# Optimization experiments

Measured on AMD Instinct MI355X. Metric: run time of the kernel, lower is better.

Reference implementation:

```python
import jax, jax.numpy as jnp
import numpy as np

H = 16          # num_attention_heads
D = 1024        # hidden_size
HD = D // H     # attention_head_size = 64


def setup_inputs() -> dict:
    key = jax.random.key(0)
    ks = jax.random.split(key, 9)
    s = 1.0 / np.sqrt(D)
    return {
        "hidden_states": jax.random.normal(ks[0], (4, 1024, D), jnp.float32),
        "encoder_hidden_states": jax.random.normal(ks[1], (4, 1024, D), jnp.float32),
        "attention_mask": jnp.zeros((4, 1, 1, 2048), jnp.float32),
        "Wq": jax.random.normal(ks[2], (D, D), jnp.float32) * s,
        "bq": jnp.zeros((D,), jnp.float32),
        "Wk": jax.random.normal(ks[3], (D, D), jnp.float32) * s,
        "bk": jnp.zeros((D,), jnp.float32),
        "Wv": jax.random.normal(ks[4], (D, D), jnp.float32) * s,
        "bv": jnp.zeros((D,), jnp.float32),
    }


def _split_heads(x):
    # [B, S, D] -> [B, H, S, HD]
    B, S, _ = x.shape
    return x.reshape(B, S, H, HD).transpose(0, 2, 1, 3)


def reference(hidden_states, encoder_hidden_states, attention_mask, Wq, bq, Wk, bk, Wv, bv):
    # KV over concat(encoder, decoder); Q over decoder hidden states only.
    all_hidden = jnp.concatenate([encoder_hidden_states, hidden_states], axis=1)  # [B, Skv, D]
    q = _split_heads(hidden_states @ Wq + bq)        # [B, H, Sq, HD]
    k = _split_heads(all_hidden @ Wk + bk)           # [B, H, Skv, HD]
    v = _split_heads(all_hidden @ Wv + bv)           # [B, H, Skv, HD]

    scores = jnp.einsum("bhqd,bhkd->bhqk", q, k) / np.sqrt(HD).astype(np.float32)
    scores = scores + attention_mask                 # additive mask, broadcast
    probs = jax.nn.softmax(scores, axis=-1)          # dropout p=0 (eval)
    ctx = jnp.einsum("bhqk,bhkd->bhqd", probs, v)    # [B, H, Sq, HD]
    B, _, Sq, _ = ctx.shape
    return ctx.transpose(0, 2, 1, 3).reshape(B, Sq, D)
```

## Files before the change

### kernel.cpp

```cpp
#include <hip/hip_runtime.h>


typedef _Float16 f16;
typedef __attribute__((ext_vector_type(4))) _Float16 half4;
typedef __attribute__((ext_vector_type(8))) _Float16 half8;
typedef __attribute__((ext_vector_type(4))) float floatx4;
typedef __attribute__((ext_vector_type(16))) float floatx16;
typedef __attribute__((ext_vector_type(4))) unsigned int uint4v;

#define GLOAD16(gp, lp)                                                        \
    __builtin_amdgcn_global_load_lds(                                          \
        (const __attribute__((address_space(1))) void*)(gp),                   \
        (__attribute__((address_space(3))) void*)(lp), 16, 0, 0)

__global__ void prep_kernel(const float* __restrict__ hid, const float* __restrict__ enc,
                            const float* __restrict__ Wq, const float* __restrict__ Wk,
                            const float* __restrict__ Wv, f16* __restrict__ Wtq,
                            f16* __restrict__ Wtk, f16* __restrict__ Wtv,
                            f16* __restrict__ Aall) {
    int bid = blockIdx.x, tid = threadIdx.x;
    if (bid < 3072) {
        __shared__ float tile[32][33];
        int z = bid >> 10, xy = bid & 1023;
        const float* W = (z == 0) ? Wq : (z == 1) ? Wk : Wv;
        f16* Wt = (z == 0) ? Wtq : (z == 1) ? Wtk : Wtv;
        int n0 = (xy & 31) * 32, k0 = (xy >> 5) * 32;
        int tx = tid & 31, ty = tid >> 5;
        #pragma unroll
        for (int i = 0; i < 32; i += 8)
            tile[ty + i][tx] = W[(k0 + ty + i) * 1024 + n0 + tx];
        __syncthreads();
        #pragma unroll
        for (int i = 0; i < 32; i += 8)
            Wt[(n0 + ty + i) * 1024 + k0 + tx] = (f16)tile[tx][ty + i];
    } else {
        int t = (bid - 3072) * 256 + tid;
        int rowg = t >> 7, col = (t & 127) * 8;
        int b = rowg >> 11, r = rowg & 2047;
        const float* src = (r < 1024 ? enc + ((size_t)b * 1024 + r) * 1024
                                     : hid + ((size_t)b * 1024 + (r - 1024)) * 1024) + col;
        float4 v0 = *(const float4*)src, v1 = *(const float4*)(src + 4);
        half8 o;
        o[0] = (f16)v0.x; o[1] = (f16)v0.y; o[2] = (f16)v0.z; o[3] = (f16)v0.w;
        o[4] = (f16)v1.x; o[5] = (f16)v1.y; o[6] = (f16)v1.z; o[7] = (f16)v1.w;
        *(half8*)(Aall + (size_t)rowg * 1024 + col) = o;
    }
}

__launch_bounds__(256)
__global__ void qkv_gemm(const f16* __restrict__ Aall,
                         const f16* __restrict__ Wtq, const f16* __restrict__ Wtk,
                         const f16* __restrict__ Wtv,
                         const float* __restrict__ bq, const float* __restrict__ bk,
                         const float* __restrict__ bv,
                         f16* __restrict__ Qw, f16* __restrict__ Kw, f16* __restrict__ Vtw) {
    int mode = blockIdx.z;
    if (mode == 0 && blockIdx.x >= 32) return;
    __shared__ f16 As0[128 * 32];
    __shared__ f16 Bs0[128 * 32];
    __shared__ f16 As1[128 * 32];
    __shared__ f16 Bs1[128 * 32];

    const f16* Wt = (mode == 0) ? Wtq : (mode == 1) ? Wtk : Wtv;
    const float* bias = (mode == 0) ? bq : (mode == 1) ? bk : bv;
    f16* out = (mode == 0) ? Qw : (mode == 1) ? Kw : Vtw;

    int tid = threadIdx.x;
    int m0 = blockIdx.x * 128, n0 = blockIdx.y * 128;
    int wid = tid >> 6, lane = tid & 63;
    int wm = (wid >> 1) * 64, wn = (wid & 1) * 64;
    int lr = lane & 15, lg = lane >> 4;

    floatx4 acc[4][4];
    #pragma unroll
    for (int i = 0; i < 4; i++)
        #pragma unroll
        for (int j = 0; j < 4; j++) acc[i][j] = (floatx4)(0.f);

    int trow = tid >> 2;
    int tcol = (((tid & 3) ^ ((tid >> 3) & 3))) * 8;
    const f16 *a0g, *a1g;
    {
        int mA0 = m0 + trow, mA1 = mA0 + 64;
        if (mode == 0) {
            int b0 = mA0 >> 10, b1 = mA1 >> 10;
            a0g = Aall + ((size_t)(b0 * 2048 + 1024 + (mA0 & 1023))) * 1024 + tcol;
            a1g = Aall + ((size_t)(b1 * 2048 + 1024 + (mA1 & 1023))) * 1024 + tcol;
        } else {
            a0g = Aall + (size_t)mA0 * 1024 + tcol;
            a1g = Aall + (size_t)mA1 * 1024 + tcol;
        }
    }
    const f16* b0g = Wt + (size_t)(n0 + trow) * 1024 + tcol;
    const f16* b1g = Wt + (size_t)(n0 + trow + 64) * 1024 + tcol;

    int rcol = (lg ^ ((lr >> 1) & 3)) * 8;

    GLOAD16(a0g, &As0[tid * 8]);
    GLOAD16(a1g, &As0[tid * 8 + 2048]);
    GLOAD16(b0g, &Bs0[tid * 8]);
    GLOAD16(b1g, &Bs0[tid * 8 + 2048]);
    GLOAD16(a0g + 32, &As1[tid * 8]);
    GLOAD16(a1g + 32, &As1[tid * 8 + 2048]);
    GLOAD16(b0g + 32, &Bs1[tid * 8]);
    GLOAD16(b1g + 32, &Bs1[tid * 8 + 2048]);
    asm volatile("s_waitcnt vmcnt(4)" ::: "memory");
    __builtin_amdgcn_s_barrier();

    #define QKV_COMPUTE(Abuf, Bbuf)                                                       \
        {                                                                                 \
            half8 a[4], bf[4];                                                            \
            _Pragma("unroll")                                                             \
            for (int i = 0; i < 4; i++)                                                   \
                a[i] = *(const half8*)&Abuf[(wm + i * 16 + lr) * 32 + rcol];              \
            _Pragma("unroll")                                                             \
            for (int j = 0; j < 4; j++)                                                   \
                bf[j] = *(const half8*)&Bbuf[(wn + j * 16 + lr) * 32 + rcol];             \
            __builtin_amdgcn_s_setprio(1);                                                \
            _Pragma("unroll")                                                             \
            for (int i = 0; i < 4; i++)                                                   \
                _Pragma("unroll")                                                         \
                for (int j = 0; j < 4; j++)                                               \
                    acc[i][j] = __builtin_amdgcn_mfma_f32_16x16x32_f16(a[i], bf[j],       \
                                                                      acc[i][j], 0, 0, 0);\
            __builtin_amdgcn_s_setprio(0);                                                \
        }

    for (int k0 = 0; k0 < 1024; k0 += 64) {
        QKV_COMPUTE(As0, Bs0);
        asm volatile("s_waitcnt lgkmcnt(0)" ::: "memory");
        __builtin_amdgcn_s_barrier();
        if (k0 + 64 < 1024) {
            GLOAD16(a0g + k0 + 64, &As0[tid * 8]);
            GLOAD16(a1g + k0 + 64, &As0[tid * 8 + 2048]);
            GLOAD16(b0g + k0 + 64, &Bs0[tid * 8]);
            GLOAD16(b1g + k0 + 64, &Bs0[tid * 8 + 2048]);
            asm volatile("s_waitcnt vmcnt(4)" ::: "memory");
        } else {
            asm volatile("s_waitcnt vmcnt(0)" ::: "memory");
        }
        __builtin_amdgcn_s_barrier();

        QKV_COMPUTE(As1, Bs1);
        asm volatile("s_waitcnt lgkmcnt(0)" ::: "memory");
        __builtin_amdgcn_s_barrier();
        if (k0 + 96 < 1024) {
            GLOAD16(a0g + k0 + 96, &As1[tid * 8]);
            GLOAD16(a1g + k0 + 96, &As1[tid * 8 + 2048]);
            GLOAD16(b0g + k0 + 96, &Bs1[tid * 8]);
            GLOAD16(b1g + k0 + 96, &Bs1[tid * 8 + 2048]);
            asm volatile("s_waitcnt vmcnt(4)" ::: "memory");
            __builtin_amdgcn_s_barrier();
        }
    }
    #undef QKV_COMPUTE

    if (mode == 2) {
        #pragma unroll
        for (int i = 0; i < 4; i++) {
            int mbase = m0 + wm + i * 16 + lg * 4;
            int b = mbase >> 11, s = mbase & 2047;
            #pragma unroll
            for (int j = 0; j < 4; j++) {
                int n = n0 + wn + j * 16 + lr;
                int h = n >> 6, d = n & 63;
                float bv = bias[n];
                half4 w;
                #pragma unroll
                for (int r = 0; r < 4; r++) w[r] = (f16)(acc[i][j][r] + bv);
                *(half4*)(out + ((size_t)((b * 16 + h) * 64 + d)) * 2048 + s) = w;
            }
        }
    } else {
        int Sout = (mode == 0) ? 1024 : 2048;
        #pragma unroll
        for (int i = 0; i < 4; i++) {
            int mbase = m0 + wm + i * 16 + lg * 4;
            #pragma unroll
            for (int j = 0; j < 4; j++) {
                int n = n0 + wn + j * 16 + lr;
                int h = n >> 6, d = n & 63;
                float bv = bias[n];
                #pragma unroll
                for (int r = 0; r < 4; r++) {
                    int m = mbase + r;
                    int b = (mode == 0) ? (m >> 10) : (m >> 11);
                    int s = (mode == 0) ? (m & 1023) : (m & 2047);
                    out[((size_t)(b * 16 + h) * Sout + s) * 64 + d] = (f16)(acc[i][j][r] + bv);
                }
            }
        }
    }
}

__device__ inline half8 pack_swap(float s0, float s1, float s2, float s3,
                                  float s4, float s5, float s6, float s7) {
    unsigned a0 = __builtin_bit_cast(unsigned, __builtin_amdgcn_cvt_pkrtz(s0, s1));
    unsigned b0 = __builtin_bit_cast(unsigned, __builtin_amdgcn_cvt_pkrtz(s4, s5));
    unsigned a1 = __builtin_bit_cast(unsigned, __builtin_amdgcn_cvt_pkrtz(s2, s3));
    unsigned b1 = __builtin_bit_cast(unsigned, __builtin_amdgcn_cvt_pkrtz(s6, s7));
    asm("v_permlane32_swap_b32 %0, %1" : "+v"(a0), "+v"(b0));
    asm("v_permlane32_swap_b32 %0, %1" : "+v"(a1), "+v"(b1));
    uint4v w = {a0, a1, b0, b1};
    return __builtin_bit_cast(half8, w);
}

__device__ inline half8 pack_noswap(float s0, float s1, float s2, float s3,
                                    float s4, float s5, float s6, float s7) {
    unsigned w0 = __builtin_bit_cast(unsigned, __builtin_amdgcn_cvt_pkrtz(s0, s1));
    unsigned w1 = __builtin_bit_cast(unsigned, __builtin_amdgcn_cvt_pkrtz(s2, s3));
    unsigned w2 = __builtin_bit_cast(unsigned, __builtin_amdgcn_cvt_pkrtz(s4, s5));
    unsigned w3 = __builtin_bit_cast(unsigned, __builtin_amdgcn_cvt_pkrtz(s6, s7));
    uint4v w = {w0, w1, w2, w3};
    return __builtin_bit_cast(half8, w);
}

__launch_bounds__(256)
__global__ void attn_kernel(const f16* __restrict__ Q, const f16* __restrict__ K,
                            const f16* __restrict__ Vt, const float* __restrict__ mask,
                            float* __restrict__ out) {
    __shared__ f16 Kt[2][64 * 72];
    __shared__ f16 Vtt[2][64 * 72];
    __shared__ float maskLds[2048];

    const float LOG2E = 1.4426950408889634f;
    int tid = threadIdx.x;
    int wid = tid >> 6, lane = tid & 63;
    int l31 = lane & 31, l5 = lane >> 5;

    int bid = blockIdx.x + 8 * blockIdx.y;
    int xcd = bid & 7, w = bid >> 3;
    int bh = xcd * 8 + (w >> 3);
    int xblk = w & 7;
    int b = bh >> 4;
    int q = xblk * 128 + wid * 32 + l31;

    half8 pa, pcode;
    #pragma unroll
    for (int j = 0; j < 8; j++) { pa[j] = (f16)0; pcode[j] = (f16)(8 * l5 + j); }
    if (l31 < 16 && (l31 >> 3) == l5) pa[l31 & 7] = (f16)1;
    floatx16 pd = __builtin_amdgcn_mfma_f32_32x32x16_f16(pa, pcode, (floatx16)0.f, 0, 0, 0);
    float r4 = __shfl(pd[0], 32);
    bool twoblk = (r4 > 6.0f);

    const float* maskp = mask + b * 2048;
    for (int i = tid; i < 512; i += 256) {
        float4 mv = ((const float4*)maskp)[i];
        mv.x = mv.x * LOG2E - 8.0f; mv.y = mv.y * LOG2E - 8.0f;
        mv.z = mv.z * LOG2E - 8.0f; mv.w = mv.w * LOG2E - 8.0f;
        ((float4*)maskLds)[i] = mv;
    }

    const f16* qrow = Q + ((size_t)bh * 1024 + q) * 64;
    half8 qf[4];
    if (!twoblk) {
        #pragma unroll
        for (int ks = 0; ks < 4; ks++)
            qf[ks] = *(const half8*)(qrow + ks * 16 + l5 * 8);
    } else {
        #pragma unroll
        for (int ks = 0; ks < 4; ks++) {
            half4 lo = *(const half4*)(qrow + ks * 16 + 4 * l5);
            half4 hi = *(const half4*)(qrow + ks * 16 + 8 + 4 * l5);
            qf[ks][0] = lo[0]; qf[ks][1] = lo[1]; qf[ks][2] = lo[2]; qf[ks][3] = lo[3];
            qf[ks][4] = hi[0]; qf[ks][5] = hi[1]; qf[ks][6] = hi[2]; qf[ks][7] = hi[3];
        }
    }
    const f16 qs = (f16)(0.125f * 1.4426950408889634f);
    #pragma unroll
    for (int ks = 0; ks < 4; ks++)
        #pragma unroll
        for (int x = 0; x < 8; x++) qf[ks][x] *= qs;

    half8 aones;
    #pragma unroll
    for (int j = 0; j < 8; j++) aones[j] = (l31 == 0) ? (f16)1 : (f16)0;

    floatx16 o0 = (floatx16)0.f, o1 = (floatx16)0.f, o2 = (floatx16)0.f;

    int sr = tid >> 2, sc = (tid & 3) * 16;
    const f16* Ksrc = K + ((size_t)bh * 2048 + sr) * 64 + sc;
    const f16* Vsrc = Vt + ((size_t)(bh * 64 + sr)) * 2048 + sc;

    half8 rk0 = *(const half8*)(Ksrc);
    half8 rk1 = *(const half8*)(Ksrc + 8);
    half8 rv0 = *(const half8*)(Vsrc);
    half8 rv1 = *(const half8*)(Vsrc + 8);
    *(half8*)&Kt[0][sr * 72 + sc]      = rk0;
    *(half8*)&Kt[0][sr * 72 + sc + 8]  = rk1;
    *(half8*)&Vtt[0][sr * 72 + sc]     = rv0;
    *(half8*)&Vtt[0][sr * 72 + sc + 8] = rv1;
    rk0 = *(const half8*)(Ksrc + (size_t)64 * 64);
    rk1 = *(const half8*)(Ksrc + (size_t)64 * 64 + 8);
    rv0 = *(const half8*)(Vsrc + 64);
    rv1 = *(const half8*)(Vsrc + 64 + 8);
    __syncthreads();

    int cur = 0;
    for (int kv0 = 0; kv0 < 2048; kv0 += 64) {
        if (kv0 < 2048 - 64) {
            int nx = cur ^ 1;
            *(half8*)&Kt[nx][sr * 72 + sc]      = rk0;
            *(half8*)&Kt[nx][sr * 72 + sc + 8]  = rk1;
            *(half8*)&Vtt[nx][sr * 72 + sc]     = rv0;
            *(half8*)&Vtt[nx][sr * 72 + sc + 8] = rv1;
            if (kv0 < 2048 - 128) {
                rk0 = *(const half8*)(Ksrc + (size_t)(kv0 + 128) * 64);
                rk1 = *(const half8*)(Ksrc + (size_t)(kv0 + 128) * 64 + 8);
                rv0 = *(const half8*)(Vsrc + kv0 + 128);
                rv1 = *(const half8*)(Vsrc + kv0 + 128 + 8);
            }
        }

        floatx16 sf0, sf1;
        #pragma unroll
        for (int g = 0; g < 4; g++) {
            float4 mk0 = *(const float4*)&maskLds[kv0 + 8 * g + 4 * l5];
            float4 mk1 = *(const float4*)&maskLds[kv0 + 32 + 8 * g + 4 * l5];
            #pragma unroll
            for (int i = 0; i < 4; i++) {
                sf0[4 * g + i] = ((const float*)&mk0)[i];
                sf1[4 * g + i] = ((const float*)&mk1)[i];
            }
        }

        __builtin_amdgcn_s_setprio(1);
        #pragma unroll
        for (int ks = 0; ks < 4; ks++) {
            half8 k0 = *(const half8*)&Kt[cur][l31 * 72 + ks * 16 + l5 * 8];
            half8 k1 = *(const half8*)&Kt[cur][(32 + l31) * 72 + ks * 16 + l5 * 8];
            sf0 = __builtin_amdgcn_mfma_f32_32x32x16_f16(k0, qf[ks], sf0, 0, 0, 0);
            sf1 = __builtin_amdgcn_mfma_f32_32x32x16_f16(k1, qf[ks], sf1, 0, 0, 0);
        }
        __builtin_amdgcn_s_setprio(0);

        #pragma unroll
        for (int r = 0; r < 16; r++) {
            sf0[r] = exp2f(sf0[r]);
            sf1[r] = exp2f(sf1[r]);
        }

        half8 pb[4];
        if (!twoblk) {
            pb[0] = pack_swap(sf0[0], sf0[1], sf0[2], sf0[3], sf0[4], sf0[5], sf0[6], sf0[7]);
            pb[1] = pack_swap(sf0[8], sf0[9], sf0[10], sf0[11], sf0[12], sf0[13], sf0[14], sf0[15]);
            pb[2] = pack_swap(sf1[0], sf1[1], sf1[2], sf1[3], sf1[4], sf1[5], sf1[6], sf1[7]);
            pb[3] = pack_swap(sf1[8], sf1[9], sf1[10], sf1[11], sf1[12], sf1[13], sf1[14], sf1[15]);
        } else {
            pb[0] = pack_noswap(sf0[0], sf0[1], sf0[2], sf0[3], sf0[4], sf0[5], sf0[6], sf0[7]);
            pb[1] = pack_noswap(sf0[8], sf0[9], sf0[10], sf0[11], sf0[12], sf0[13], sf0[14], sf0[15]);
            pb[2] = pack_noswap(sf1[0], sf1[1], sf1[2], sf1[3], sf1[4], sf1[5], sf1[6], sf1[7]);
            pb[3] = pack_noswap(sf1[8], sf1[9], sf1[10], sf1[11], sf1[12], sf1[13], sf1[14], sf1[15]);
        }

        __builtin_amdgcn_s_setprio(1);
        #pragma unroll
        for (int kb = 0; kb < 4; kb++) {
            half8 v0 = *(const half8*)&Vtt[cur][l31 * 72 + kb * 16 + l5 * 8];
            half8 v1 = *(const half8*)&Vtt[cur][(32 + l31) * 72 + kb * 16 + l5 * 8];
            o0 = __builtin_amdgcn_mfma_f32_32x32x16_f16(v0, pb[kb], o0, 0, 0, 0);
            o1 = __builtin_amdgcn_mfma_f32_32x32x16_f16(v1, pb[kb], o1, 0, 0, 0);
            o2 = __builtin_amdgcn_mfma_f32_32x32x16_f16(aones, pb[kb], o2, 0, 0, 0);
        }
        __builtin_amdgcn_s_setprio(0);

        asm volatile("s_waitcnt lgkmcnt(0)" ::: "memory");
        __builtin_amdgcn_sched_barrier(0);
        __builtin_amdgcn_s_barrier();
        cur ^= 1;
    }

    float l_all = __shfl(o2[0], l31);
    int h = bh & 15;
    float inv = 1.f / l_all;
    float* orow = out + ((size_t)(b * 1024 + q)) * 1024 + h * 64;
    #pragma unroll
    for (int g = 0; g < 4; g++) {
        float4 r0 = {o0[4 * g] * inv, o0[4 * g + 1] * inv, o0[4 * g + 2] * inv, o0[4 * g + 3] * inv};
        float4 r1 = {o1[4 * g] * inv, o1[4 * g + 1] * inv, o1[4 * g + 2] * inv, o1[4 * g + 3] * inv};
        *(float4*)&orow[8 * g + 4 * l5]      = r0;
        *(float4*)&orow[32 + 8 * g + 4 * l5] = r1;
    }
}

extern "C" void kernel_launch(void* const* d_in, const int* in_sizes, int n_in,
                              void* d_out, int out_size, void* d_ws, size_t ws_size,
                              hipStream_t stream) {
    const float* hid  = (const float*)d_in[0];
    const float* enc  = (const float*)d_in[1];
    const float* mask = (const float*)d_in[2];
    const float* Wq   = (const float*)d_in[3];
    const float* bq   = (const float*)d_in[4];
    const float* Wk   = (const float*)d_in[5];
    const float* bk   = (const float*)d_in[6];
    const float* Wv   = (const float*)d_in[7];
    const float* bv   = (const float*)d_in[8];
    float* out = (float*)d_out;

    char* ws = (char*)d_ws;
    f16* Wtq  = (f16*)(ws + ((size_t)0 << 20));
    f16* Wtk  = (f16*)(ws + ((size_t)2 << 20));
    f16* Wtv  = (f16*)(ws + ((size_t)4 << 20));
    f16* Aall = (f16*)(ws + ((size_t)6 << 20));
    f16* Qw   = (f16*)(ws + ((size_t)22 << 20));
    f16* Kw   = (f16*)(ws + ((size_t)30 << 20));
    f16* Vtw  = (f16*)(ws + ((size_t)46 << 20));

    prep_kernel<<<7168, 256, 0, stream>>>(hid, enc, Wq, Wk, Wv, Wtq, Wtk, Wtv, Aall);

    qkv_gemm<<<dim3(64, 8, 3), 256, 0, stream>>>(Aall, Wtq, Wtk, Wtv, bq, bk, bv, Qw, Kw, Vtw);

    attn_kernel<<<dim3(8, 64), 256, 0, stream>>>(Qw, Kw, Vtw, mask, out);
}
```

Measured before the change: 143.6 us.

## Triple-buffer QKV GEMM LDS tiles to deepen async load pipeline

Adds a third pair of LDS buffers to the QKV projection GEMM, giving a three-stage global_load_lds pipeline with two tiles in flight instead of one. The main loop now steps 96 along K, with a two-tile epilogue that handles the remaining 64. The aim is to hide more global memory latency behind the MFMA work. In exchange, LDS use per block grows by half, which could cut occupancy.

After: 142.9 us (median of 2 runs). About the same (-0.5%).

```diff
diff --git a/kernel.cpp b/kernel.cpp
--- a/kernel.cpp
+++ b/kernel.cpp
@@ -60,6 +60,8 @@
     __shared__ f16 Bs0[128 * 32];
     __shared__ f16 As1[128 * 32];
     __shared__ f16 Bs1[128 * 32];
+    __shared__ f16 As2[128 * 32];
+    __shared__ f16 Bs2[128 * 32];
 
     const f16* Wt = (mode == 0) ? Wtq : (mode == 1) ? Wtk : Wtv;
     const float* bias = (mode == 0) ? bq : (mode == 1) ? bk : bv;
@@ -96,16 +98,11 @@
 
     int rcol = (lg ^ ((lr >> 1) & 3)) * 8;
 
-    GLOAD16(a0g, &As0[tid * 8]);
-    GLOAD16(a1g, &As0[tid * 8 + 2048]);
-    GLOAD16(b0g, &Bs0[tid * 8]);
-    GLOAD16(b1g, &Bs0[tid * 8 + 2048]);
-    GLOAD16(a0g + 32, &As1[tid * 8]);
-    GLOAD16(a1g + 32, &As1[tid * 8 + 2048]);
-    GLOAD16(b0g + 32, &Bs1[tid * 8]);
-    GLOAD16(b1g + 32, &Bs1[tid * 8 + 2048]);
-    asm volatile("s_waitcnt vmcnt(4)" ::: "memory");
-    __builtin_amdgcn_s_barrier();
+    #define QKV_STAGE(off, Abuf, Bbuf)                    \
+        GLOAD16(a0g + (off), &Abuf[tid * 8]);             \
+        GLOAD16(a1g + (off), &Abuf[tid * 8 + 2048]);      \
+        GLOAD16(b0g + (off), &Bbuf[tid * 8]);             \
+        GLOAD16(b1g + (off), &Bbuf[tid * 8 + 2048]);
 
     #define QKV_COMPUTE(Abuf, Bbuf)                                                       \
         {                                                                                 \
@@ -126,33 +123,45 @@
             __builtin_amdgcn_s_setprio(0);                                                \
         }
 
-    for (int k0 = 0; k0 < 1024; k0 += 64) {
+    QKV_STAGE(0,  As0, Bs0);
+    QKV_STAGE(32, As1, Bs1);
+    QKV_STAGE(64, As2, Bs2);
+    asm volatile("s_waitcnt vmcnt(8)" ::: "memory");
+    __builtin_amdgcn_s_barrier();
+
+    for (int k0 = 0; k0 < 960; k0 += 96) {
         QKV_COMPUTE(As0, Bs0);
         asm volatile("s_waitcnt lgkmcnt(0)" ::: "memory");
         __builtin_amdgcn_s_barrier();
-        if (k0 + 64 < 1024) {
-            GLOAD16(a0g + k0 + 64, &As0[tid * 8]);
-            GLOAD16(a1g + k0 + 64, &As0[tid * 8 + 2048]);
-            GLOAD16(b0g + k0 + 64, &Bs0[tid * 8]);
-            GLOAD16(b1g + k0 + 64, &Bs0[tid * 8 + 2048]);
-            asm volatile("s_waitcnt vmcnt(4)" ::: "memory");
-        } else {
-            asm volatile("s_waitcnt vmcnt(0)" ::: "memory");
-        }
+        QKV_STAGE(k0 + 96, As0, Bs0);
+        asm volatile("s_waitcnt vmcnt(8)" ::: "memory");
         __builtin_amdgcn_s_barrier();
 
         QKV_COMPUTE(As1, Bs1);
         asm volatile("s_waitcnt lgkmcnt(0)" ::: "memory");
         __builtin_amdgcn_s_barrier();
-        if (k0 + 96 < 1024) {
-            GLOAD16(a0g + k0 + 96, &As1[tid * 8]);
-            GLOAD16(a1g + k0 + 96, &As1[tid * 8 + 2048]);
-            GLOAD16(b0g + k0 + 96, &Bs1[tid * 8]);
-            GLOAD16(b1g + k0 + 96, &Bs1[tid * 8 + 2048]);
+        QKV_STAGE(k0 + 128, As1, Bs1);
+        asm volatile("s_waitcnt vmcnt(8)" ::: "memory");
+        __builtin_amdgcn_s_barrier();
+
+        QKV_COMPUTE(As2, Bs2);
+        asm volatile("s_waitcnt lgkmcnt(0)" ::: "memory");
+        __builtin_amdgcn_s_barrier();
+        if (k0 + 160 < 1024) {
+            QKV_STAGE(k0 + 160, As2, Bs2);
+            asm volatile("s_waitcnt vmcnt(8)" ::: "memory");
+        } else {
             asm volatile("s_waitcnt vmcnt(4)" ::: "memory");
-            __builtin_amdgcn_s_barrier();
-        }
-    }
+        }
+        __builtin_amdgcn_s_barrier();
+    }
+
+    QKV_COMPUTE(As0, Bs0);
+    asm volatile("s_waitcnt vmcnt(0)" ::: "memory");
+    __builtin_amdgcn_s_barrier();
+    QKV_COMPUTE(As1, Bs1);
+
+    #undef QKV_STAGE
     #undef QKV_COMPUTE
 
     if (mode == 2) {
```
